# Performance work log

Measured on AMD Instinct MI355X. Metric: run time of the kernel, lower is better.

## Reference

```python
import jax, jax.numpy as jnp
import numpy as np

K = 10          # number of neighbors (init kwarg k)
NUM_CLASSES = 100  # label vocabulary (targets drawn in [0, 100))


def setup_inputs() -> dict:
    key = jax.random.key(0)
    k1, k2, k3 = jax.random.split(key, 3)
    X = jax.random.normal(k1, (1024, 512), dtype=jnp.float32)
    data = jax.random.normal(k2, (50000, 512), dtype=jnp.float32)
    targets = jax.random.randint(k3, (50000,), 0, NUM_CLASSES, dtype=jnp.int64)
    return {"X": X, "data": data, "targets": targets}


def reference(X, data, targets):
    # Pairwise L2 distance (p=2 path of the module), computed via the
    x2 = jnp.sum(X * X, axis=1, keepdims=True)              # [Q, 1]
    d2 = jnp.sum(data * data, axis=1)                        # [N]
    sq = x2 + d2[None, :] - 2.0 * (X @ data.T)               # [Q, N]
    dist = jnp.sqrt(jnp.maximum(sq, 0.0))                    # torch.norm(p1-p2, p=2)

    # torch: sort distances ascending, take first k indices -> top-k smallest.
    _, idx = jax.lax.top_k(-dist, K)                         # [Q, K]
    labels = targets[idx]                                    # [Q, K]

    # torch.mode over the k neighbor labels: histogram + argmax.
    # argmax picks the first (smallest) class on ties, matching torch.mode.
    counts = jax.nn.one_hot(labels, NUM_CLASSES, dtype=jnp.float32).sum(axis=1)  # [Q, C]
    pred = jnp.argmax(counts, axis=1).astype(jnp.float32)    # [Q]
    return pred
```

## Files before the change

kernel.cpp:

```cpp
#include <hip/hip_runtime.h>
#include <math.h>
#include <limits.h>

#define QN 1024
#define NN 50000
#define NPAD 50048
#define DD 512
#define KNN 10
#define NT 128
#define QTB 128
#define BK 32
#define NS 391
#define QB 8
#define NSAMP 31
#define NREST (NS - NSAMP)
#define CAP 512

#define WS_D2  0
#define WS_TAU 50048
#define WS_CNT (WS_TAU + 2048)
#define WS_XH  (WS_CNT + 1024)
#define WS_XL  (WS_XH + QN * DD / 2)
#define WS_CKS (WS_XL + QN * DD / 2)
#define WS_BUF (WS_CKS + QN * NSAMP * KNN * 2)
#define WS_DH  (WS_BUF + QN * CAP * 2)
#define WS_DL  (WS_DH + NS * 16 * 2048)
#define WS_END (WS_DL + NS * 16 * 2048)

typedef __attribute__((ext_vector_type(8))) short short8;
typedef __attribute__((ext_vector_type(4))) float f32x4;
typedef unsigned long long u64;

__device__ __forceinline__ u64 mkkey(float f, int idx) {
  unsigned u = __float_as_uint(f);
  unsigned m = u ^ ((unsigned)((int)u >> 31) | 0x80000000u);
  return ((u64)m << 32) | (unsigned)idx;
}

__device__ __forceinline__ void cvt2(float x, float y, unsigned& hi, unsigned& lo) {
  unsigned ux = __float_as_uint(x), uy = __float_as_uint(y);
  unsigned rx = ux + 0x7fffu + ((ux >> 16) & 1u);
  unsigned ry = uy + 0x7fffu + ((uy >> 16) & 1u);
  hi = (rx >> 16) | (ry & 0xffff0000u);
  float xl = x - __uint_as_float(rx & 0xffff0000u);
  float yl = y - __uint_as_float(ry & 0xffff0000u);
  unsigned uxl = __float_as_uint(xl), uyl = __float_as_uint(yl);
  unsigned rxl = uxl + 0x7fffu + ((uxl >> 16) & 1u);
  unsigned ryl = uyl + 0x7fffu + ((uyl >> 16) & 1u);
  lo = (rxl >> 16) | (ryl & 0xffff0000u);
}

__device__ __forceinline__ void glds16(const void* g, void* l) {
  __builtin_amdgcn_global_load_lds(
      (const __attribute__((address_space(1))) unsigned*)g,
      (__attribute__((address_space(3))) unsigned*)l, 16, 0, 0);
}

__device__ __forceinline__ void ins10(u64* kl, u64 k) {
#pragma unroll
  for (int u = 0; u < KNN; u++) {
    u64 lo = (k < kl[u]) ? k : kl[u];
    u64 hi = (k < kl[u]) ? kl[u] : k;
    kl[u] = lo; k = hi;
  }
}

__global__ __launch_bounds__(256) void convx_kernel(
    const float* __restrict__ Xm, float* __restrict__ ws) {
  const int g = blockIdx.x * 256 + threadIdx.x;
  const int b = g >> 10, kc = (g >> 6) & 15, l = g & 63;
  const int row = b * 16 + (l & 15);
  const int col = kc * 32 + (l >> 4) * 8;
  const float4* p = (const float4*)(Xm + (size_t)row * DD + col);
  float4 v0 = p[0], v1 = p[1];
  unsigned h[4], lo[4];
  cvt2(v0.x, v0.y, h[0], lo[0]); cvt2(v0.z, v0.w, h[1], lo[1]);
  cvt2(v1.x, v1.y, h[2], lo[2]); cvt2(v1.z, v1.w, h[3], lo[3]);
  ((uint4*)(ws + WS_XH))[g] = make_uint4(h[0], h[1], h[2], h[3]);
  ((uint4*)(ws + WS_XL))[g] = make_uint4(lo[0], lo[1], lo[2], lo[3]);
}

__global__ __launch_bounds__(256) void convd_kernel(
    const float* __restrict__ dat, float* __restrict__ ws) {
  const int slice = blockIdx.x;
  const int t = threadIdx.x;
  const int row = t >> 1, h2 = t & 1;
  const int gr = slice * NT + row;
  const int r15 = row & 15;
  float s = 0.f;
#pragma unroll
  for (int kc8 = 0; kc8 < 8; kc8++) {
    const int kc = h2 * 8 + kc8;
    float4 v[8];
    if (gr < NN) {
      const float4* src = (const float4*)(dat + (size_t)gr * DD + kc * 32);
#pragma unroll
      for (int j = 0; j < 8; j++) v[j] = src[j];
    } else {
#pragma unroll
      for (int j = 0; j < 8; j++) v[j] = make_float4(0.f, 0.f, 0.f, 0.f);
    }
    unsigned hw[16], lw[16];
#pragma unroll
    for (int j = 0; j < 8; j++) {
      s = fmaf(v[j].x, v[j].x, s); s = fmaf(v[j].y, v[j].y, s);
      s = fmaf(v[j].z, v[j].z, s); s = fmaf(v[j].w, v[j].w, s);
      cvt2(v[j].x, v[j].y, hw[2 * j], lw[2 * j]);
      cvt2(v[j].z, v[j].w, hw[2 * j + 1], lw[2 * j + 1]);
    }
    uint4* dhp = (uint4*)((unsigned char*)(ws + WS_DH) +
                          (((size_t)slice * 16 + kc) * 8 + (row >> 4)) * 1024);
    uint4* dlp = (uint4*)((unsigned char*)(ws + WS_DL) +
                          (((size_t)slice * 16 + kc) * 8 + (row >> 4)) * 1024);
#pragma unroll
    for (int qd = 0; qd < 4; qd++) {
      dhp[qd * 16 + r15] = make_uint4(hw[4 * qd], hw[4 * qd + 1], hw[4 * qd + 2], hw[4 * qd + 3]);
      dlp[qd * 16 + r15] = make_uint4(lw[4 * qd], lw[4 * qd + 1], lw[4 * qd + 2], lw[4 * qd + 3]);
    }
  }
  s += __shfl_xor(s, 1, 64);
  if (h2 == 0) ws[WS_D2 + gr] = (gr < NN) ? s : __builtin_inff();
}

struct StageT { unsigned char bh[8192], bl[8192]; };
struct EpiT  { float sq[64][132]; };
struct ListT { u64 kl[64][4][KNN]; };

template <int MODE> struct SmemSel {
  union U { StageT s; EpiT e; ListT l; };
};
template <> struct SmemSel<1> {
  struct U { StageT s; u64 tau[128]; };
};

template <int PRE, int MODE>
__global__ __launch_bounds__(256, 3) void knn_chunk(
    const float* __restrict__ dat, float* __restrict__ ws, int soff) {
  __shared__ __align__(16) typename SmemSel<MODE>::U sm;
  int bqx, bsy;
  if (MODE == 1 && (gridDim.y & 7) == 0) {
    const int n = (int)(blockIdx.y * gridDim.x + blockIdx.x);
    const int m = n >> 3;
    const int ypx = (int)(gridDim.y >> 3);
    bqx = m & 7;
    bsy = (n & 7) * ypx + (m >> 3);
  } else {
    bqx = blockIdx.x; bsy = blockIdx.y;
  }
  const int qbase = bqx * QTB;
  const int slice = bsy + soff;
  const int nbase = slice * NT;
  const int t = threadIdx.x;
  const int lane = t & 63, wave = t >> 6;
  const int wn = wave & 1, wq = wave >> 1;
  const unsigned char* dh = (const unsigned char*)(ws + WS_DH);
  const unsigned char* dl = (const unsigned char*)(ws + WS_DL);
  const char* xfh = (const char*)(ws + WS_XH);
  const char* xfl = (const char*)(ws + WS_XL);
  const int abase = (((bqx * 8 + wq * 4) * 16) * 64 + lane) * 16;

  f32x4 acc[4][4];
#pragma unroll
  for (int i = 0; i < 4; i++)
#pragma unroll
    for (int j = 0; j < 4; j++) acc[i][j] = (f32x4)0.f;

  auto stageB = [&](int kc) {
#pragma unroll
    for (int i = 0; i < 4; i++) {
      int pp = wave * 4 + i;
      int p = pp & 7;
      const unsigned char* g = (pp < 8 ? dh : dl) +
          (((size_t)slice * 16 + kc) * 8 + p) * 1024 + lane * 16;
      glds16(g, (pp < 8 ? sm.s.bh : sm.s.bl) + p * 1024);
    }
  };

  if (PRE) {
    stageB(0);
    for (int kc = 0; kc < 16; kc++) {
      short8 fah[4], fal[4];
#pragma unroll
      for (int i = 0; i < 4; i++) {
        int off = abase + (i * 1024 + kc * 64) * 16;
        fah[i] = *(const short8*)(xfh + off);
        fal[i] = *(const short8*)(xfl + off);
      }
      __syncthreads();
      const int fragoff = lane * 16;
      short8 fbh[4], fbl[4];
#pragma unroll
      for (int i = 0; i < 4; i++) {
        fbh[i] = *(const short8*)(sm.s.bh + (wn * 4 + i) * 1024 + fragoff);
        fbl[i] = *(const short8*)(sm.s.bl + (wn * 4 + i) * 1024 + fragoff);
      }
      __syncthreads();
      if (kc < 15) stageB(kc + 1);
#pragma unroll
      for (int mt = 0; mt < 4; mt++)
#pragma unroll
        for (int nt = 0; nt < 4; nt++)
          acc[mt][nt] = __builtin_amdgcn_mfma_f32_16x16x32_bf16(fah[mt], fbh[nt], acc[mt][nt], 0, 0, 0);
#pragma unroll
      for (int mt = 0; mt < 4; mt++)
#pragma unroll
        for (int nt = 0; nt < 4; nt++)
          acc[mt][nt] = __builtin_amdgcn_mfma_f32_16x16x32_bf16(fah[mt], fbl[nt], acc[mt][nt], 0, 0, 0);
#pragma unroll
      for (int mt = 0; mt < 4; mt++)
#pragma unroll
        for (int nt = 0; nt < 4; nt++)
          acc[mt][nt] = __builtin_amdgcn_mfma_f32_16x16x32_bf16(fal[mt], fbh[nt], acc[mt][nt], 0, 0, 0);
    }
  } else {
    const int brow = t >> 1, bh_half = t & 1;
    const int bgr = nbase + brow;
    const int bpanel = (brow >> 4) * 1024;
    const int bchunk = (brow & 15) * 16;
    for (int kc = 0; kc < 16; kc++) {
      const int kk = kc * BK;
      short8 fah[4], fal[4];
#pragma unroll
      for (int i = 0; i < 4; i++) {
        int off = abase + (i * 1024 + kc * 64) * 16;
        fah[i] = *(const short8*)(xfh + off);
        fal[i] = *(const short8*)(xfl + off);
      }
      __syncthreads();
      {
        float4 v0 = make_float4(0.f, 0.f, 0.f, 0.f), v1 = v0, v2 = v0, v3 = v0;
        if (bgr < NN) {
          const float4* src = (const float4*)(dat + (size_t)bgr * DD + kk + bh_half * 16);
          v0 = src[0]; v1 = src[1]; v2 = src[2]; v3 = src[3];
        }
        unsigned hw[8], lw[8];
        cvt2(v0.x, v0.y, hw[0], lw[0]); cvt2(v0.z, v0.w, hw[1], lw[1]);
        cvt2(v1.x, v1.y, hw[2], lw[2]); cvt2(v1.z, v1.w, hw[3], lw[3]);
        cvt2(v2.x, v2.y, hw[4], lw[4]); cvt2(v2.z, v2.w, hw[5], lw[5]);
        cvt2(v3.x, v3.y, hw[6], lw[6]); cvt2(v3.z, v3.w, hw[7], lw[7]);
        unsigned char* bhp = sm.s.bh + bpanel;
        unsigned char* blp = sm.s.bl + bpanel;
        *(uint4*)(bhp + (2 * bh_half) * 256 + bchunk)     = make_uint4(hw[0], hw[1], hw[2], hw[3]);
        *(uint4*)(bhp + (2 * bh_half + 1) * 256 + bchunk) = make_uint4(hw[4], hw[5], hw[6], hw[7]);
        *(uint4*)(blp + (2 * bh_half) * 256 + bchunk)     = make_uint4(lw[0], lw[1], lw[2], lw[3]);
        *(uint4*)(blp + (2 * bh_half + 1) * 256 + bchunk) = make_uint4(lw[4], lw[5], lw[6], lw[7]);
      }
      __syncthreads();
      const int fragoff = lane * 16;
      short8 fbh[4], fbl[4];
#pragma unroll
      for (int i = 0; i < 4; i++) {
        fbh[i] = *(const short8*)(sm.s.bh + (wn * 4 + i) * 1024 + fragoff);
        fbl[i] = *(const short8*)(sm.s.bl + (wn * 4 + i) * 1024 + fragoff);
      }
      __syncthreads();
#pragma unroll
      for (int mt = 0; mt < 4; mt++)
#pragma unroll
        for (int nt = 0; nt < 4; nt++) {
          acc[mt][nt] = __builtin_amdgcn_mfma_f32_16x16x32_bf16(fah[mt], fbh[nt], acc[mt][nt], 0, 0, 0);
          acc[mt][nt] = __builtin_amdgcn_mfma_f32_16x16x32_bf16(fah[mt], fbl[nt], acc[mt][nt], 0, 0, 0);
          acc[mt][nt] = __builtin_amdgcn_mfma_f32_16x16x32_bf16(fal[mt], fbh[nt], acc[mt][nt], 0, 0, 0);
        }
    }
  }

  if constexpr (MODE == 0) {
#pragma unroll
    for (int pass = 0; pass < 2; pass++) {
      __syncthreads();
      if (wq == pass) {
#pragma unroll
        for (int nt = 0; nt < 4; nt++) {
          int col = wn * 64 + nt * 16 + (lane & 15);
          float d2v = ws[WS_D2 + nbase + col];
#pragma unroll
          for (int mt = 0; mt < 4; mt++)
#pragma unroll
            for (int rg = 0; rg < 4; rg++) {
              int lr = mt * 16 + (lane >> 4) * 4 + rg;
              sm.e.sq[lr][col] = fmaf(-2.f, acc[mt][nt][rg], d2v);
            }
        }
      }
      __syncthreads();
      {
        const int r = t >> 2, s = t & 3;
        u64 kl[KNN];
#pragma unroll
        for (int u = 0; u < KNN; u++) kl[u] = ~0ull;
        for (int jj = 0; jj < 32; jj++) {
          int c = s * 32 + ((jj + r + 8 * s) & 31);
          float v = sm.e.sq[r][c];
          ins10(kl, mkkey(v, nbase + c));
        }
        __syncthreads();
#pragma unroll
        for (int u = 0; u < KNN; u++) sm.l.kl[r][s][u] = kl[u];
      }
      __syncthreads();
      if (t < 64) {
        u64* dst = ((u64*)(ws + WS_CKS)) +
                   ((size_t)(qbase + pass * 64 + t) * NSAMP + blockIdx.y) * KNN;
        int h0 = 0, h1 = 0, h2 = 0, h3 = 0;
        for (int pick = 0; pick < KNN; pick++) {
          u64 k0 = sm.l.kl[t][0][h0], k1 = sm.l.kl[t][1][h1];
          u64 k2 = sm.l.kl[t][2][h2], k3 = sm.l.kl[t][3][h3];
          u64 best = k0; int bm = 0;
          if (k1 < best) { best = k1; bm = 1; }
          if (k2 < best) { best = k2; bm = 2; }
          if (k3 < best) { best = k3; bm = 3; }
          dst[pick] = best;
          h0 += (bm == 0); h1 += (bm == 1); h2 += (bm == 2); h3 += (bm == 3);
        }
      }
    }
  } else {
    if (t < 128) sm.tau[t] = ((const u64*)(ws + WS_TAU))[qbase + t];
    __syncthreads();
    unsigned* cnt = (unsigned*)(ws + WS_CNT);
    u64* buf = (u64*)(ws + WS_BUF);
    float d2v[4];
#pragma unroll
    for (int nt = 0; nt < 4; nt++)
      d2v[nt] = ws[WS_D2 + nbase + wn * 64 + nt * 16 + (lane & 15)];
#pragma unroll
    for (int mt = 0; mt < 4; mt++)
#pragma unroll
      for (int rg = 0; rg < 4; rg++) {
        int row = wq * 64 + mt * 16 + (lane >> 4) * 4 + rg;
        u64 tr = sm.tau[row];
#pragma unroll
        for (int nt = 0; nt < 4; nt++) {
          float d = fmaf(-2.f, acc[mt][nt][rg], d2v[nt]);
          int col = nbase + wn * 64 + nt * 16 + (lane & 15);
          u64 key = mkkey(d, col);
          if (key < tr) {
            int q = qbase + row;
            unsigned slot = atomicAdd(cnt + q, 1u);
            if (slot < CAP) buf[(size_t)q * CAP + slot] = key;
          }
        }
      }
  }
}

__global__ __launch_bounds__(64) void tau_kernel(float* __restrict__ ws) {
  const int q = blockIdx.x;
  const int t = threadIdx.x;
  const u64* samp = ((const u64*)(ws + WS_CKS)) + (size_t)q * NSAMP * KNN;
  const int NC = NSAMP * KNN;
  u64 kl[KNN];
#pragma unroll
  for (int u = 0; u < KNN; u++) kl[u] = ~0ull;
  for (int j = t; j < NC; j += 64) ins10(kl, samp[j]);
  __shared__ u64 wk[64][KNN];
  __shared__ u64 m2[8][KNN];
#pragma unroll
  for (int u = 0; u < KNN; u++) wk[t][u] = kl[u];
  __syncthreads();
  if (t < 8) {
    int h[8] = {0, 0, 0, 0, 0, 0, 0, 0};
    for (int pick = 0; pick < KNN; pick++) {
      u64 best = ~0ull; int bm = 0;
#pragma unroll
      for (int m = 0; m < 8; m++) {
        u64 km = wk[t * 8 + m][h[m]];
        if (km < best) { best = km; bm = m; }
      }
      m2[t][pick] = best;
#pragma unroll
      for (int m = 0; m < 8; m++) h[m] += (bm == m);
    }
  }
  __syncthreads();
  if (t == 0) {
    int h[8] = {0, 0, 0, 0, 0, 0, 0, 0};
    u64 best = 0;
    for (int pick = 0; pick < KNN; pick++) {
      best = ~0ull; int bm = 0;
#pragma unroll
      for (int m = 0; m < 8; m++) {
        u64 km = m2[m][h[m]];
        if (km < best) { best = km; bm = m; }
      }
#pragma unroll
      for (int m = 0; m < 8; m++) h[m] += (bm == m);
    }
    ((u64*)(ws + WS_TAU))[q] = best;
    ((unsigned*)(ws + WS_CNT))[q] = 0u;
  }
}

__global__ __launch_bounds__(64) void knn_final(
    const int* __restrict__ targets, float* __restrict__ ws,
    float* __restrict__ out) {
  const int q = blockIdx.x;
  const int t = threadIdx.x;
  const u64* samp = ((const u64*)(ws + WS_CKS)) + (size_t)q * NSAMP * KNN;
  const u64* buf = ((const u64*)(ws + WS_BUF)) + (size_t)q * CAP;
  unsigned c = ((const unsigned*)(ws + WS_CNT))[q];
  if (c > CAP) c = CAP;

  u64 kl[KNN];
#pragma unroll
  for (int u = 0; u < KNN; u++) kl[u] = ~0ull;
  for (int j = t; j < NSAMP * KNN; j += 64) ins10(kl, samp[j]);
  for (int j = t; j < (int)c; j += 64) ins10(kl, buf[j]);

  __shared__ u64 wk[64][KNN];
  __shared__ u64 m2[8][KNN];
#pragma unroll
  for (int u = 0; u < KNN; u++) wk[t][u] = kl[u];
  __syncthreads();
  if (t < 8) {
    int h[8] = {0, 0, 0, 0, 0, 0, 0, 0};
    for (int pick = 0; pick < KNN; pick++) {
      u64 best = ~0ull; int bm = 0;
#pragma unroll
      for (int m = 0; m < 8; m++) {
        u64 km = wk[t * 8 + m][h[m]];
        if (km < best) { best = km; bm = m; }
      }
      m2[t][pick] = best;
#pragma unroll
      for (int m = 0; m < 8; m++) h[m] += (bm == m);
    }
  }
  __syncthreads();
  if (t == 0) {
    int h[8] = {0, 0, 0, 0, 0, 0, 0, 0};
    int fi[KNN];
    for (int pick = 0; pick < KNN; pick++) {
      u64 best = ~0ull; int bm = 0;
#pragma unroll
      for (int m = 0; m < 8; m++) {
        u64 km = m2[m][h[m]];
        if (km < best) { best = km; bm = m; }
      }
      fi[pick] = (int)(unsigned)(best & 0xffffffffu);
#pragma unroll
      for (int m = 0; m < 8; m++) h[m] += (bm == m);
    }
    int lab[KNN];
#pragma unroll
    for (int u = 0; u < KNN; u++) lab[u] = targets[fi[u]];
    int bc = 0, bl = INT_MAX;
#pragma unroll
    for (int i = 0; i < KNN; i++) {
      int cc = 0;
#pragma unroll
      for (int j = 0; j < KNN; j++) cc += (lab[j] == lab[i]) ? 1 : 0;
      if (cc > bc || (cc == bc && lab[i] < bl)) { bc = cc; bl = lab[i]; }
    }
    out[q] = (float)bl;
  }
}

extern "C" void kernel_launch(void* const* d_in, const int* in_sizes, int n_in,
                              void* d_out, int out_size, void* d_ws, size_t ws_size,
                              hipStream_t stream) {
  const float* Xm  = (const float*)d_in[0];
  const float* dat = (const float*)d_in[1];
  const int* targets = (const int*)d_in[2];
  float* out = (float*)d_out;
  float* ws  = (float*)d_ws;
  const bool pre = ws_size >= (size_t)WS_END * 4;

  hipLaunchKernelGGL(convx_kernel, dim3(QN * DD / 8 / 256), dim3(256), 0, stream, Xm, ws);
  hipLaunchKernelGGL(convd_kernel, dim3(NS), dim3(256), 0, stream, dat, ws);
  if (pre) {
    hipLaunchKernelGGL((knn_chunk<1, 0>), dim3(QB, NSAMP), dim3(256), 0, stream, dat, ws, 0);
    hipLaunchKernelGGL(tau_kernel, dim3(QN), dim3(64), 0, stream, ws);
    hipLaunchKernelGGL((knn_chunk<1, 1>), dim3(QB, NREST), dim3(256), 0, stream, dat, ws, NSAMP);
  } else {
    hipLaunchKernelGGL((knn_chunk<0, 0>), dim3(QB, NSAMP), dim3(256), 0, stream, dat, ws, 0);
    hipLaunchKernelGGL(tau_kernel, dim3(QN), dim3(64), 0, stream, ws);
    hipLaunchKernelGGL((knn_chunk<0, 1>), dim3(QB, NREST), dim3(256), 0, stream, dat, ws, NSAMP);
  }
  hipLaunchKernelGGL(knn_final, dim3(QN), dim3(64), 0, stream, targets, ws, out);
}
```

Before: 363.9 us.

## Use single bf16 GEMM for candidate filtering with fp32 exact rerank

```diff
diff --git a/kernel.cpp b/kernel.cpp
--- a/kernel.cpp
+++ b/kernel.cpp
@@ -12,20 +12,20 @@
 #define BK 32
 #define NS 391
 #define QB 8
-#define NSAMP 31
+#define NSAMP 63
 #define NREST (NS - NSAMP)
 #define CAP 512
+#define SLACK 4.0f
+#define LCAP 1152
 
 #define WS_D2  0
 #define WS_TAU 50048
-#define WS_CNT (WS_TAU + 2048)
+#define WS_CNT (WS_TAU + 1024)
 #define WS_XH  (WS_CNT + 1024)
-#define WS_XL  (WS_XH + QN * DD / 2)
-#define WS_CKS (WS_XL + QN * DD / 2)
+#define WS_CKS (WS_XH + QN * DD / 2)
 #define WS_BUF (WS_CKS + QN * NSAMP * KNN * 2)
 #define WS_DH  (WS_BUF + QN * CAP * 2)
-#define WS_DL  (WS_DH + NS * 16 * 2048)
-#define WS_END (WS_DL + NS * 16 * 2048)
+#define WS_END (WS_DH + NS * 16 * 2048)
 
 typedef __attribute__((ext_vector_type(8))) short short8;
 typedef __attribute__((ext_vector_type(4))) float f32x4;
@@ -37,17 +37,16 @@
   return ((u64)m << 32) | (unsigned)idx;
 }
 
-__device__ __forceinline__ void cvt2(float x, float y, unsigned& hi, unsigned& lo) {
+__device__ __forceinline__ float keyhi_f(unsigned m) {
+  unsigned u = (m & 0x80000000u) ? (m ^ 0x80000000u) : ~m;
+  return __uint_as_float(u);
+}
+
+__device__ __forceinline__ unsigned cvth(float x, float y) {
   unsigned ux = __float_as_uint(x), uy = __float_as_uint(y);
   unsigned rx = ux + 0x7fffu + ((ux >> 16) & 1u);
   unsigned ry = uy + 0x7fffu + ((uy >> 16) & 1u);
-  hi = (rx >> 16) | (ry & 0xffff0000u);
-  float xl = x - __uint_as_float(rx & 0xffff0000u);
-  float yl = y - __uint_as_float(ry & 0xffff0000u);
-  unsigned uxl = __float_as_uint(xl), uyl = __float_as_uint(yl);
-  unsigned rxl = uxl + 0x7fffu + ((uxl >> 16) & 1u);
-  unsigned ryl = uyl + 0x7fffu + ((uyl >> 16) & 1u);
-  lo = (rxl >> 16) | (ryl & 0xffff0000u);
+  return (rx >> 16) | (ry & 0xffff0000u);
 }
 
 __device__ __forceinline__ void glds16(const void* g, void* l) {
@@ -65,23 +64,20 @@
   }
 }
 
-__global__ __launch_bounds__(256) void convx_kernel(
-    const float* __restrict__ Xm, float* __restrict__ ws) {
-  const int g = blockIdx.x * 256 + threadIdx.x;
-  const int b = g >> 10, kc = (g >> 6) & 15, l = g & 63;
-  const int row = b * 16 + (l & 15);
-  const int col = kc * 32 + (l >> 4) * 8;
-  const float4* p = (const float4*)(Xm + (size_t)row * DD + col);
-  float4 v0 = p[0], v1 = p[1];
-  unsigned h[4], lo[4];
-  cvt2(v0.x, v0.y, h[0], lo[0]); cvt2(v0.z, v0.w, h[1], lo[1]);
-  cvt2(v1.x, v1.y, h[2], lo[2]); cvt2(v1.z, v1.w, h[3], lo[3]);
-  ((uint4*)(ws + WS_XH))[g] = make_uint4(h[0], h[1], h[2], h[3]);
-  ((uint4*)(ws + WS_XL))[g] = make_uint4(lo[0], lo[1], lo[2], lo[3]);
-}
-
-__global__ __launch_bounds__(256) void convd_kernel(
-    const float* __restrict__ dat, float* __restrict__ ws) {
+__global__ __launch_bounds__(256) void conv_kernel(
+    const float* __restrict__ dat, const float* __restrict__ Xm,
+    float* __restrict__ ws) {
+  if ((int)blockIdx.x >= NS) {
+    const int g = ((int)blockIdx.x - NS) * 256 + threadIdx.x;
+    const int b = g >> 10, kc = (g >> 6) & 15, l = g & 63;
+    const int row = b * 16 + (l & 15);
+    const int col = kc * 32 + (l >> 4) * 8;
+    const float4* p = (const float4*)(Xm + (size_t)row * DD + col);
+    float4 v0 = p[0], v1 = p[1];
+    ((uint4*)(ws + WS_XH))[g] = make_uint4(
+        cvth(v0.x, v0.y), cvth(v0.z, v0.w), cvth(v1.x, v1.y), cvth(v1.z, v1.w));
+    return;
+  }
   const int slice = blockIdx.x;
   const int t = threadIdx.x;
   const int row = t >> 1, h2 = t & 1;
@@ -100,29 +96,25 @@
 #pragma unroll
       for (int j = 0; j < 8; j++) v[j] = make_float4(0.f, 0.f, 0.f, 0.f);
     }
-    unsigned hw[16], lw[16];
+    unsigned hw[16];
 #pragma unroll
     for (int j = 0; j < 8; j++) {
       s = fmaf(v[j].x, v[j].x, s); s = fmaf(v[j].y, v[j].y, s);
       s = fmaf(v[j].z, v[j].z, s); s = fmaf(v[j].w, v[j].w, s);
-      cvt2(v[j].x, v[j].y, hw[2 * j], lw[2 * j]);
-      cvt2(v[j].z, v[j].w, hw[2 * j + 1], lw[2 * j + 1]);
+      hw[2 * j]     = cvth(v[j].x, v[j].y);
+      hw[2 * j + 1] = cvth(v[j].z, v[j].w);
     }
     uint4* dhp = (uint4*)((unsigned char*)(ws + WS_DH) +
                           (((size_t)slice * 16 + kc) * 8 + (row >> 4)) * 1024);
-    uint4* dlp = (uint4*)((unsigned char*)(ws + WS_DL) +
-                          (((size_t)slice * 16 + kc) * 8 + (row >> 4)) * 1024);
-#pragma unroll
-    for (int qd = 0; qd < 4; qd++) {
+#pragma unroll
+    for (int qd = 0; qd < 4; qd++)
       dhp[qd * 16 + r15] = make_uint4(hw[4 * qd], hw[4 * qd + 1], hw[4 * qd + 2], hw[4 * qd + 3]);
-      dlp[qd * 16 + r15] = make_uint4(lw[4 * qd], lw[4 * qd + 1], lw[4 * qd + 2], lw[4 * qd + 3]);
-    }
   }
   s += __shfl_xor(s, 1, 64);
   if (h2 == 0) ws[WS_D2 + gr] = (gr < NN) ? s : __builtin_inff();
 }
 
-struct StageT { unsigned char bh[8192], bl[8192]; };
+struct StageT { unsigned char bh[8192]; };
 struct EpiT  { float sq[64][132]; };
 struct ListT { u64 kl[64][4][KNN]; };
 
@@ -130,7 +122,7 @@
   union U { StageT s; EpiT e; ListT l; };
 };
 template <> struct SmemSel<1> {
-  struct U { StageT s; u64 tau[128]; };
+  struct U { StageT s; float tau[128]; };
 };
 
 template <int PRE, int MODE>
@@ -154,9 +146,7 @@
   const int lane = t & 63, wave = t >> 6;
   const int wn = wave & 1, wq = wave >> 1;
   const unsigned char* dh = (const unsigned char*)(ws + WS_DH);
-  const unsigned char* dl = (const unsigned char*)(ws + WS_DL);
   const char* xfh = (const char*)(ws + WS_XH);
-  const char* xfl = (const char*)(ws + WS_XL);
   const int abase = (((bqx * 8 + wq * 4) * 16) * 64 + lane) * 16;
 
   f32x4 acc[4][4];
@@ -167,33 +157,27 @@
 
   auto stageB = [&](int kc) {
 #pragma unroll
-    for (int i = 0; i < 4; i++) {
-      int pp = wave * 4 + i;
-      int p = pp & 7;
-      const unsigned char* g = (pp < 8 ? dh : dl) +
+    for (int i = 0; i < 2; i++) {
+      int p = wave * 2 + i;
+      const unsigned char* g = dh +
           (((size_t)slice * 16 + kc) * 8 + p) * 1024 + lane * 16;
-      glds16(g, (pp < 8 ? sm.s.bh : sm.s.bl) + p * 1024);
+      glds16(g, sm.s.bh + p * 1024);
     }
   };
 
   if (PRE) {
     stageB(0);
     for (int kc = 0; kc < 16; kc++) {
-      short8 fah[4], fal[4];
-#pragma unroll
-      for (int i = 0; i < 4; i++) {
-        int off = abase + (i * 1024 + kc * 64) * 16;
-        fah[i] = *(const short8*)(xfh + off);
-        fal[i] = *(const short8*)(xfl + off);
-      }
+      short8 fah[4];
+#pragma unroll
+      for (int i = 0; i < 4; i++)
+        fah[i] = *(const short8*)(xfh + abase + i * 16384 + kc * 1024);
       __syncthreads();
       const int fragoff = lane * 16;
-      short8 fbh[4], fbl[4];
-#pragma unroll
-      for (int i = 0; i < 4; i++) {
+      short8 fbh[4];
+#pragma unroll
+      for (int i = 0; i < 4; i++)
         fbh[i] = *(const short8*)(sm.s.bh + (wn * 4 + i) * 1024 + fragoff);
-        fbl[i] = *(const short8*)(sm.s.bl + (wn * 4 + i) * 1024 + fragoff);
-      }
       __syncthreads();
       if (kc < 15) stageB(kc + 1);
 #pragma unroll
@@ -201,16 +185,6 @@
 #pragma unroll
         for (int nt = 0; nt < 4; nt++)
           acc[mt][nt] = __builtin_amdgcn_mfma_f32_16x16x32_bf16(fah[mt], fbh[nt], acc[mt][nt], 0, 0, 0);
-#pragma unroll
-      for (int mt = 0; mt < 4; mt++)
-#pragma unroll
-        for (int nt = 0; nt < 4; nt++)
-          acc[mt][nt] = __builtin_amdgcn_mfma_f32_16x16x32_bf16(fah[mt], fbl[nt], acc[mt][nt], 0, 0, 0);
-#pragma unroll
-      for (int mt = 0; mt < 4; mt++)
-#pragma unroll
-        for (int nt = 0; nt < 4; nt++)
-          acc[mt][nt] = __builtin_amdgcn_mfma_f32_16x16x32_bf16(fal[mt], fbh[nt], acc[mt][nt], 0, 0, 0);
     }
   } else {
     const int brow = t >> 1, bh_half = t & 1;
@@ -219,13 +193,10 @@
     const int bchunk = (brow & 15) * 16;
     for (int kc = 0; kc < 16; kc++) {
       const int kk = kc * BK;
-      short8 fah[4], fal[4];
-#pragma unroll
-      for (int i = 0; i < 4; i++) {
-        int off = abase + (i * 1024 + kc * 64) * 16;
-        fah[i] = *(const short8*)(xfh + off);
-        fal[i] = *(const short8*)(xfl + off);
-      }
+      short8 fah[4];
+#pragma unroll
+      for (int i = 0; i < 4; i++)
+        fah[i] = *(const short8*)(xfh + abase + i * 16384 + kc * 1024);
       __syncthreads();
       {
         float4 v0 = make_float4(0.f, 0.f, 0.f, 0.f), v1 = v0, v2 = v0, v3 = v0;
@@ -233,35 +204,24 @@
           const float4* src = (const float4*)(dat + (size_t)bgr * DD + kk + bh_half * 16);
           v0 = src[0]; v1 = src[1]; v2 = src[2]; v3 = src[3];
         }
-        unsigned hw[8], lw[8];
-        cvt2(v0.x, v0.y, hw[0], lw[0]); cvt2(v0.z, v0.w, hw[1], lw[1]);
-        cvt2(v1.x, v1.y, hw[2], lw[2]); cvt2(v1.z, v1.w, hw[3], lw[3]);
-        cvt2(v2.x, v2.y, hw[4], lw[4]); cvt2(v2.z, v2.w, hw[5], lw[5]);
-        cvt2(v3.x, v3.y, hw[6], lw[6]); cvt2(v3.z, v3.w, hw[7], lw[7]);
         unsigned char* bhp = sm.s.bh + bpanel;
-        unsigned char* blp = sm.s.bl + bpanel;
-        *(uint4*)(bhp + (2 * bh_half) * 256 + bchunk)     = make_uint4(hw[0], hw[1], hw[2], hw[3]);
-        *(uint4*)(bhp + (2 * bh_half + 1) * 256 + bchunk) = make_uint4(hw[4], hw[5], hw[6], hw[7]);
-        *(uint4*)(blp + (2 * bh_half) * 256 + bchunk)     = make_uint4(lw[0], lw[1], lw[2], lw[3]);
-        *(uint4*)(blp + (2 * bh_half + 1) * 256 + bchunk) = make_uint4(lw[4], lw[5], lw[6], lw[7]);
+        *(uint4*)(bhp + (2 * bh_half) * 256 + bchunk) =
+            make_uint4(cvth(v0.x, v0.y), cvth(v0.z, v0.w), cvth(v1.x, v1.y), cvth(v1.z, v1.w));
+        *(uint4*)(bhp + (2 * bh_half + 1) * 256 + bchunk) =
+            make_uint4(cvth(v2.x, v2.y), cvth(v2.z, v2.w), cvth(v3.x, v3.y), cvth(v3.z, v3.w));
       }
       __syncthreads();
       const int fragoff = lane * 16;
-      short8 fbh[4], fbl[4];
-#pragma unroll
-      for (int i = 0; i < 4; i++) {
+      short8 fbh[4];
+#pragma unroll
+      for (int i = 0; i < 4; i++)
         fbh[i] = *(const short8*)(sm.s.bh + (wn * 4 + i) * 1024 + fragoff);
-        fbl[i] = *(const short8*)(sm.s.bl + (wn * 4 + i) * 1024 + fragoff);
-      }
       __syncthreads();
 #pragma unroll
       for (int mt = 0; mt < 4; mt++)
 #pragma unroll
-        for (int nt = 0; nt < 4; nt++) {
+        for (int nt = 0; nt < 4; nt++)
           acc[mt][nt] = __builtin_amdgcn_mfma_f32_16x16x32_bf16(fah[mt], fbh[nt], acc[mt][nt], 0, 0, 0);
-          acc[mt][nt] = __builtin_amdgcn_mfma_f32_16x16x32_bf16(fah[mt], fbl[nt], acc[mt][nt], 0, 0, 0);
-          acc[mt][nt] = __builtin_amdgcn_mfma_f32_16x16x32_bf16(fal[mt], fbh[nt], acc[mt][nt], 0, 0, 0);
-        }
     }
   }
 
@@ -316,7 +276,7 @@
       }
     }
   } else {
-    if (t < 128) sm.tau[t] = ((const u64*)(ws + WS_TAU))[qbase + t];
+    if (t < 128) sm.tau[t] = ws[WS_TAU + qbase + t];
     __syncthreads();
     unsigned* cnt = (unsigned*)(ws + WS_CNT);
     u64* buf = (u64*)(ws + WS_BUF);
@@ -329,16 +289,15 @@
 #pragma unroll
       for (int rg = 0; rg < 4; rg++) {
         int row = wq * 64 + mt * 16 + (lane >> 4) * 4 + rg;
-        u64 tr = sm.tau[row];
+        float tr = sm.tau[row];
 #pragma unroll
         for (int nt = 0; nt < 4; nt++) {
           float d = fmaf(-2.f, acc[mt][nt][rg], d2v[nt]);
-          int col = nbase + wn * 64 + nt * 16 + (lane & 15);
-          u64 key = mkkey(d, col);
-          if (key < tr) {
+          if (d < tr) {
+            int col = nbase + wn * 64 + nt * 16 + (lane & 15);
             int q = qbase + row;
             unsigned slot = atomicAdd(cnt + q, 1u);
-            if (slot < CAP) buf[(size_t)q * CAP + slot] = key;
+            if (slot < CAP) buf[(size_t)q * CAP + slot] = mkkey(d, col);
           }
         }
       }
@@ -387,60 +346,78 @@
 #pragma unroll
       for (int m = 0; m < 8; m++) h[m] += (bm == m);
     }
-    ((u64*)(ws + WS_TAU))[q] = best;
+    ws[WS_TAU + q] = keyhi_f((unsigned)(best >> 32)) + SLACK;
     ((unsigned*)(ws + WS_CNT))[q] = 0u;
   }
 }
 
-__global__ __launch_bounds__(64) void knn_final(
-    const int* __restrict__ targets, float* __restrict__ ws,
+__global__ __launch_bounds__(256) void knn_final(
+    const int* __restrict__ targets, const float* __restrict__ Xm,
+    const float* __restrict__ dat, float* __restrict__ ws,
     float* __restrict__ out) {
   const int q = blockIdx.x;
   const int t = threadIdx.x;
+  const int lane = t & 63, wave = t >> 6;
+  __shared__ float qrow[DD];
+  __shared__ unsigned lst[LCAP];
+  __shared__ int nlist;
+  __shared__ u64 wk4[4][KNN];
+  if (t == 0) nlist = 0;
+  if (t < 128) ((float4*)qrow)[t] = ((const float4*)(Xm + (size_t)q * DD))[t];
+  __syncthreads();
+  const float tr = ws[WS_TAU + q];
   const u64* samp = ((const u64*)(ws + WS_CKS)) + (size_t)q * NSAMP * KNN;
-  const u64* buf = ((const u64*)(ws + WS_BUF)) + (size_t)q * CAP;
+  for (int j = t; j < NSAMP * KNN; j += 256) {
+    u64 k = samp[j];
+    if (keyhi_f((unsigned)(k >> 32)) < tr) {
+      int s_ = atomicAdd(&nlist, 1);
+      if (s_ < LCAP) lst[s_] = (unsigned)k;
+    }
+  }
   unsigned c = ((const unsigned*)(ws + WS_CNT))[q];
   if (c > CAP) c = CAP;
+  const u64* buf = ((const u64*)(ws + WS_BUF)) + (size_t)q * CAP;
+  for (int j = t; j < (int)c; j += 256) {
+    int s_ = atomicAdd(&nlist, 1);
+    if (s_ < LCAP) lst[s_] = (unsigned)buf[j];
+  }
+  __syncthreads();
+  const int n = nlist < LCAP ? nlist : LCAP;
 
   u64 kl[KNN];
 #pragma unroll
   for (int u = 0; u < KNN; u++) kl[u] = ~0ull;
-  for (int j = t; j < NSAMP * KNN; j += 64) ins10(kl, samp[j]);
-  for (int j = t; j < (int)c; j += 64) ins10(kl, buf[j]);
-
-  __shared__ u64 wk[64][KNN];
-  __shared__ u64 m2[8][KNN];
-#pragma unroll
-  for (int u = 0; u < KNN; u++) wk[t][u] = kl[u];
-  __syncthreads();
-  if (t < 8) {
-    int h[8] = {0, 0, 0, 0, 0, 0, 0, 0};
-    for (int pick = 0; pick < KNN; pick++) {
-      u64 best = ~0ull; int bm = 0;
-#pragma unroll
-      for (int m = 0; m < 8; m++) {
-        u64 km = wk[t * 8 + m][h[m]];
-        if (km < best) { best = km; bm = m; }
-      }
-      m2[t][pick] = best;
-#pragma unroll
-      for (int m = 0; m < 8; m++) h[m] += (bm == m);
-    }
-  }
+  const float4* qv = (const float4*)qrow;
+  const float4 q0 = qv[lane * 2], q1 = qv[lane * 2 + 1];
+  for (int j = wave; j < n; j += 4) {
+    const unsigned idx = lst[j];
+    const float4* xr = (const float4*)(dat + (size_t)idx * DD) + lane * 2;
+    const float4 a0 = xr[0], a1 = xr[1];
+    float p = a0.x * q0.x;
+    p = fmaf(a0.y, q0.y, p); p = fmaf(a0.z, q0.z, p); p = fmaf(a0.w, q0.w, p);
+    p = fmaf(a1.x, q1.x, p); p = fmaf(a1.y, q1.y, p);
+    p = fmaf(a1.z, q1.z, p); p = fmaf(a1.w, q1.w, p);
+#pragma unroll
+    for (int s_ = 1; s_ < 64; s_ <<= 1) p += __shfl_xor(p, s_, 64);
+    float d = fmaf(-2.f, p, ws[WS_D2 + idx]);
+    ins10(kl, mkkey(d, (int)idx));
+  }
+  if (lane == 0)
+#pragma unroll
+    for (int u = 0; u < KNN; u++) wk4[wave][u] = kl[u];
   __syncthreads();
   if (t == 0) {
-    int h[8] = {0, 0, 0, 0, 0, 0, 0, 0};
+    int h[4] = {0, 0, 0, 0};
     int fi[KNN];
     for (int pick = 0; pick < KNN; pick++) {
       u64 best = ~0ull; int bm = 0;
 #pragma unroll
-      for (int m = 0; m < 8; m++) {
-        u64 km = m2[m][h[m]];
+      for (int m = 0; m < 4; m++) {
+        u64 km = wk4[m][h[m]];
         if (km < best) { best = km; bm = m; }
       }
       fi[pick] = (int)(unsigned)(best & 0xffffffffu);
-#pragma unroll
-      for (int m = 0; m < 8; m++) h[m] += (bm == m);
+      h[bm]++;
     }
     int lab[KNN];
 #pragma unroll
@@ -467,8 +444,8 @@
   float* ws  = (float*)d_ws;
   const bool pre = ws_size >= (size_t)WS_END * 4;
 
-  hipLaunchKernelGGL(convx_kernel, dim3(QN * DD / 8 / 256), dim3(256), 0, stream, Xm, ws);
-  hipLaunchKernelGGL(convd_kernel, dim3(NS), dim3(256), 0, stream, dat, ws);
+  hipLaunchKernelGGL(conv_kernel, dim3(NS + QN * DD / 8 / 256), dim3(256), 0,
+                     stream, dat, Xm, ws);
   if (pre) {
     hipLaunchKernelGGL((knn_chunk<1, 0>), dim3(QB, NSAMP), dim3(256), 0, stream, dat, ws, 0);
     hipLaunchKernelGGL(tau_kernel, dim3(QN), dim3(64), 0, stream, ws);
@@ -478,5 +455,5 @@
     hipLaunchKernelGGL(tau_kernel, dim3(QN), dim3(64), 0, stream, ws);
     hipLaunchKernelGGL((knn_chunk<0, 1>), dim3(QB, NREST), dim3(256), 0, stream, dat, ws, NSAMP);
   }
-  hipLaunchKernelGGL(knn_final, dim3(QN), dim3(64), 0, stream, targets, ws, out);
-}
+  hipLaunchKernelGGL(knn_final, dim3(QN), dim3(256), 0, stream, targets, Xm, dat, ws, out);
+}
```

New measurement: 317.5 us. 12.7% less time.
